# Optimization experiments

Measured on AMD Instinct MI355X. Metric: run time of the kernel, lower is better.

## Reference

```python
import jax, jax.numpy as jnp
import numpy as np

N = 50000
E = 800000
IN_C = 1024
HID = 64
HEADS = 4
OUT_C = 64
NEG_SLOPE = 0.2  # PyG GATConv default


def setup_inputs() -> dict:
    key = jax.random.key(0)
    ks = jax.random.split(key, 12)
    x = jax.random.normal(ks[0], (N, IN_C), dtype=jnp.float32)
    edge_index = jax.random.randint(ks[1], (2, E), 0, N, dtype=jnp.int64)
    s1 = 1.0 / np.sqrt(IN_C)
    s2 = 1.0 / np.sqrt(HEADS * HID)
    return {
        "x": x,
        "edge_index": edge_index,
        "W1": jax.random.normal(ks[2], (HEADS * HID, IN_C), dtype=jnp.float32) * s1,
        "a_src1": jax.random.normal(ks[3], (HEADS, HID), dtype=jnp.float32) * s2,
        "a_dst1": jax.random.normal(ks[4], (HEADS, HID), dtype=jnp.float32) * s2,
        "b1": jnp.zeros((HEADS * HID,), dtype=jnp.float32),
        "W2": jax.random.normal(ks[5], (OUT_C, HEADS * HID), dtype=jnp.float32) * s2,
        "a_src2": jax.random.normal(ks[6], (1, OUT_C), dtype=jnp.float32) * 0.1,
        "a_dst2": jax.random.normal(ks[7], (1, OUT_C), dtype=jnp.float32) * 0.1,
        "b2": jnp.zeros((OUT_C,), dtype=jnp.float32),
    }


def gat_conv(x, src, dst, W, a_src, a_dst, b, heads, concat):
    # x: [N, F_in]; src/dst: [E'] (self-loops already appended)
    n = x.shape[0]
    h = (x @ W.T).reshape(n, heads, -1)                 # [N, H, C]
    alpha_s = (h * a_src).sum(-1)                       # [N, H]
    alpha_d = (h * a_dst).sum(-1)                       # [N, H]
    e = jax.nn.leaky_relu(alpha_s[src] + alpha_d[dst], NEG_SLOPE)  # [E', H]
    # segment softmax over edges grouped by destination
    m = jax.ops.segment_max(e, dst, num_segments=n)     # [N, H]
    ex = jnp.exp(e - m[dst])
    denom = jax.ops.segment_sum(ex, dst, num_segments=n)
    alpha = ex / denom[dst]                             # [E', H]
    out = jax.ops.segment_sum(alpha[:, :, None] * h[src], dst, num_segments=n)  # [N, H, C]
    out = out.reshape(n, -1) if concat else out.mean(axis=1)
    return out + b


def reference(x, edge_index, W1, a_src1, a_dst1, b1, W2, a_src2, a_dst2, b2):
    n = x.shape[0]
    loop = jnp.arange(n, dtype=edge_index.dtype)
    src = jnp.concatenate([edge_index[0], loop])  # PyG add_self_loops=True
    dst = jnp.concatenate([edge_index[1], loop])
    # eval mode: dropout is identity
    h = gat_conv(x, src, dst, W1, a_src1, a_dst1, b1, HEADS, concat=True)
    h = jax.nn.elu(h)
    out = gat_conv(h, src, dst, W2, a_src2, a_dst2, b2, 1, concat=False)
    return out
```

## Files before the change

kernel.cpp:

```cpp
#include <hip/hip_runtime.h>
#include <hip/hip_bf16.h>
#include <math.h>

constexpr int IN_C = 1024;
constexpr int HEADS = 4;
constexpr int F1 = 256;
constexpr int OUT_C = 64;
constexpr float NEG = 0.2f;

using bf16x8 = __attribute__((ext_vector_type(8))) short;
using f32x4 = __attribute__((ext_vector_type(4))) float;

__device__ __forceinline__ float leaky(float x) { return x > 0.f ? x : NEG * x; }

__device__ __forceinline__ unsigned short bf16bits(float v) {
  __hip_bfloat16 b = __float2bfloat16(v);
  return *reinterpret_cast<unsigned short*>(&b);
}
__device__ __forceinline__ float bf2f(unsigned short u) {
  union { unsigned u; float f; } c; c.u = (unsigned)u << 16; return c.f;
}

#define GLD_LDS16(g, l)                                                        \
  __builtin_amdgcn_global_load_lds(                                            \
      (const __attribute__((address_space(1))) void*)(g),                      \
      (__attribute__((address_space(3))) void*)(l), 16, 0, 0)

__global__ void cvt_bf16_kernel(const float* __restrict__ in,
                                unsigned short* __restrict__ out, int n) {
  int i = blockIdx.x * blockDim.x + threadIdx.x;
  if (i < n) out[i] = bf16bits(in[i]);
}

constexpr int LDTA = 72;

__global__ __launch_bounds__(256, 2) void gemm1_mfma(const float* __restrict__ X,
                                                     const unsigned short* __restrict__ Wb,
                                                     unsigned short* __restrict__ Hb,
                                                     const float* __restrict__ a_src,
                                                     const float* __restrict__ a_dst,
                                                     float* __restrict__ as_out,
                                                     float* __restrict__ ad_out, int M) {
  __shared__ unsigned short As[64 * LDTA];
  __shared__ unsigned short Bs[256 * 64];
  const int tid = threadIdx.x;
  const int wave = tid >> 6;
  const int lane = tid & 63;
  const int m15 = lane & 15;
  const int q = lane >> 4;
  const int bm = blockIdx.x * 64;

  f32x4 acc[4][4];
#pragma unroll
  for (int i = 0; i < 4; ++i)
#pragma unroll
    for (int j = 0; j < 4; ++j) acc[i][j] = (f32x4){0.f, 0.f, 0.f, 0.f};

  const int ar = tid >> 2;
  const int acg = (tid & 3) * 16;
  const int agr = (bm + ar < M) ? (bm + ar) : (M - 1);
  const float* aptr = X + (size_t)agr * IN_C + acg;

  for (int kt = 0; kt < IN_C; kt += 64) {
    float4 a0 = *(const float4*)(aptr + kt + 0);
    float4 a1 = *(const float4*)(aptr + kt + 4);
    float4 a2 = *(const float4*)(aptr + kt + 8);
    float4 a3 = *(const float4*)(aptr + kt + 12);
#pragma unroll
    for (int p = 0; p < 8; ++p) {
      int s = p * 256 + tid;
      int r = s >> 3;
      int cb = s & 7;
      const unsigned short* g = Wb + (size_t)r * IN_C + kt + ((cb ^ (r & 7)) << 3);
      GLD_LDS16(g, &Bs[(p * 256 + wave * 64) * 8]);
    }
    union { uint4 u4[2]; __hip_bfloat162 h[8]; } pk;
    pk.h[0] = __float22bfloat162_rn(make_float2(a0.x, a0.y));
    pk.h[1] = __float22bfloat162_rn(make_float2(a0.z, a0.w));
    pk.h[2] = __float22bfloat162_rn(make_float2(a1.x, a1.y));
    pk.h[3] = __float22bfloat162_rn(make_float2(a1.z, a1.w));
    pk.h[4] = __float22bfloat162_rn(make_float2(a2.x, a2.y));
    pk.h[5] = __float22bfloat162_rn(make_float2(a2.z, a2.w));
    pk.h[6] = __float22bfloat162_rn(make_float2(a3.x, a3.y));
    pk.h[7] = __float22bfloat162_rn(make_float2(a3.z, a3.w));
    *(uint4*)&As[ar * LDTA + acg] = pk.u4[0];
    *(uint4*)&As[ar * LDTA + acg + 8] = pk.u4[1];
    __syncthreads();

#pragma unroll
    for (int k0 = 0; k0 < 64; k0 += 32) {
      bf16x8 af[4], bfr[4];
#pragma unroll
      for (int i = 0; i < 4; ++i)
        af[i] = *(const bf16x8*)&As[(i * 16 + m15) * LDTA + k0 + q * 8];
#pragma unroll
      for (int j = 0; j < 4; ++j) {
        int rb = wave * 64 + j * 16 + m15;
        int cbp = ((k0 >> 3) + q) ^ (rb & 7);
        bfr[j] = *(const bf16x8*)&Bs[rb * 64 + cbp * 8];
      }
#pragma unroll
      for (int i = 0; i < 4; ++i)
#pragma unroll
        for (int j = 0; j < 4; ++j)
          acc[i][j] = __builtin_amdgcn_mfma_f32_16x16x32_bf16(af[i], bfr[j], acc[i][j], 0, 0, 0);
    }
    __syncthreads();
  }
  float asf[4], adf[4];
#pragma unroll
  for (int j = 0; j < 4; ++j) {
    asf[j] = a_src[wave * 64 + j * 16 + m15];
    adf[j] = a_dst[wave * 64 + j * 16 + m15];
  }
#pragma unroll
  for (int i = 0; i < 4; ++i) {
#pragma unroll
    for (int r = 0; r < 4; ++r) {
      int row = bm + i * 16 + q * 4 + r;
      if (row < M) {
#pragma unroll
        for (int j = 0; j < 4; ++j)
          Hb[(size_t)row * F1 + wave * 64 + j * 16 + m15] = bf16bits(acc[i][j][r]);
      }
      float s = acc[i][0][r] * asf[0] + acc[i][1][r] * asf[1] +
                acc[i][2][r] * asf[2] + acc[i][3][r] * asf[3];
      float d = acc[i][0][r] * adf[0] + acc[i][1][r] * adf[1] +
                acc[i][2][r] * adf[2] + acc[i][3][r] * adf[3];
#pragma unroll
      for (int o = 1; o < 16; o <<= 1) {
        s += __shfl_xor(s, o, 64);
        d += __shfl_xor(d, o, 64);
      }
      if (m15 == 0 && row < M) {
        as_out[row * HEADS + wave] = s;
        ad_out[row * HEADS + wave] = d;
      }
    }
  }
}

__global__ __launch_bounds__(256, 4) void gemm2_mfma(const unsigned short* __restrict__ Y,
                                                     const unsigned short* __restrict__ W2b,
                                                     float* __restrict__ H2,
                                                     const float* __restrict__ a_src,
                                                     const float* __restrict__ a_dst,
                                                     float* __restrict__ as_out,
                                                     float* __restrict__ ad_out, int M) {
  __shared__ unsigned short As[64 * 64];
  __shared__ unsigned short Bs[64 * 64];
  const int tid = threadIdx.x;
  const int wave = tid >> 6;
  const int lane = tid & 63;
  const int m15 = lane & 15;
  const int q = lane >> 4;
  const int bm = blockIdx.x * 64;

  f32x4 acc[4];
#pragma unroll
  for (int j = 0; j < 4; ++j) acc[j] = (f32x4){0.f, 0.f, 0.f, 0.f};

  for (int kt = 0; kt < F1; kt += 64) {
#pragma unroll
    for (int p = 0; p < 2; ++p) {
      int s = p * 256 + tid;
      int r = s >> 3;
      int cb = s & 7;
      int colo = (cb ^ (r & 7)) << 3;
      int gr = (bm + r < M) ? (bm + r) : (M - 1);
      GLD_LDS16(Y + (size_t)gr * F1 + kt + colo, &As[(p * 256 + wave * 64) * 8]);
      GLD_LDS16(W2b + (size_t)r * F1 + kt + colo, &Bs[(p * 256 + wave * 64) * 8]);
    }
    __syncthreads();
#pragma unroll
    for (int k0 = 0; k0 < 64; k0 += 32) {
      int ra = wave * 16 + m15;
      bf16x8 af = *(const bf16x8*)&As[ra * 64 + ((((k0 >> 3) + q) ^ (ra & 7)) << 3)];
      bf16x8 bfr[4];
#pragma unroll
      for (int j = 0; j < 4; ++j) {
        int rb = j * 16 + m15;
        bfr[j] = *(const bf16x8*)&Bs[rb * 64 + ((((k0 >> 3) + q) ^ (rb & 7)) << 3)];
      }
#pragma unroll
      for (int j = 0; j < 4; ++j)
        acc[j] = __builtin_amdgcn_mfma_f32_16x16x32_bf16(af, bfr[j], acc[j], 0, 0, 0);
    }
    __syncthreads();
  }
  float asf[4], adf[4];
#pragma unroll
  for (int j = 0; j < 4; ++j) {
    asf[j] = a_src[j * 16 + m15];
    adf[j] = a_dst[j * 16 + m15];
  }
#pragma unroll
  for (int r = 0; r < 4; ++r) {
    int row = bm + wave * 16 + q * 4 + r;
    if (row < M) {
#pragma unroll
      for (int j = 0; j < 4; ++j) H2[(size_t)row * OUT_C + j * 16 + m15] = acc[j][r];
    }
    float s = acc[0][r] * asf[0] + acc[1][r] * asf[1] + acc[2][r] * asf[2] + acc[3][r] * asf[3];
    float d = acc[0][r] * adf[0] + acc[1][r] * adf[1] + acc[2][r] * adf[2] + acc[3][r] * adf[3];
#pragma unroll
    for (int o = 1; o < 16; o <<= 1) {
      s += __shfl_xor(s, o, 64);
      d += __shfl_xor(d, o, 64);
    }
    if (m15 == 0 && row < M) {
      as_out[row] = s;
      ad_out[row] = d;
    }
  }
}

__global__ void degree_kernel(const int* __restrict__ ei, int E, int N,
                              int* __restrict__ deg) {
  int e = blockIdx.x * blockDim.x + threadIdx.x;
  if (e >= E + N) return;
  int dst = (e < E) ? ei[E + e] : (e - E);
  atomicAdd(&deg[dst], 1);
}

__global__ __launch_bounds__(256) void scan_block_sums(const int* __restrict__ deg,
                                                       int* __restrict__ part, int n) {
  __shared__ int sm[256];
  int t = threadIdx.x;
  int i = blockIdx.x * 256 + t;
  sm[t] = (i < n) ? deg[i] : 0;
  __syncthreads();
  for (int off = 128; off > 0; off >>= 1) {
    if (t < off) sm[t] += sm[t + off];
    __syncthreads();
  }
  if (t == 0) part[blockIdx.x] = sm[0];
}

__global__ __launch_bounds__(256) void scan_partials(int* __restrict__ part, int P) {
  __shared__ int sm[256];
  int t = threadIdx.x;
  int v = (t < P) ? part[t] : 0;
  sm[t] = v;
  __syncthreads();
  for (int off = 1; off < 256; off <<= 1) {
    int u = (t >= off) ? sm[t - off] : 0;
    __syncthreads();
    sm[t] += u;
    __syncthreads();
  }
  if (t < P) part[t] = sm[t];
}

__global__ __launch_bounds__(256) void scan_final(const int* __restrict__ deg,
                                                  const int* __restrict__ part,
                                                  int* __restrict__ row_ptr, int n) {
  __shared__ int sm[256];
  int t = threadIdx.x;
  int i = blockIdx.x * 256 + t;
  sm[t] = (i < n) ? deg[i] : 0;
  __syncthreads();
  for (int off = 1; off < 256; off <<= 1) {
    int u = (t >= off) ? sm[t - off] : 0;
    __syncthreads();
    sm[t] += u;
    __syncthreads();
  }
  int base = blockIdx.x ? part[blockIdx.x - 1] : 0;
  if (i < n) row_ptr[i + 1] = base + sm[t];
  if (i == 0) row_ptr[0] = 0;
}

__global__ void scatter_kernel(const int* __restrict__ ei, int E, int N,
                               const int* __restrict__ row_ptr, int* __restrict__ fill,
                               int* __restrict__ col) {
  int e = blockIdx.x * blockDim.x + threadIdx.x;
  if (e >= E + N) return;
  int src, dst;
  if (e < E) { src = ei[e]; dst = ei[E + e]; }
  else       { src = e - E; dst = e - E; }
  int pos = row_ptr[dst] + atomicAdd(&fill[dst], 1);
  col[pos] = src;
}

__global__ __launch_bounds__(256) void agg1_kernel(const unsigned short* __restrict__ hb,
                                                   const float* __restrict__ as,
                                                   const float* __restrict__ ad,
                                                   const int* __restrict__ row_ptr,
                                                   const int* __restrict__ col,
                                                   const float* __restrict__ bias,
                                                   unsigned short* __restrict__ yb, int N) {
  int dst = (blockIdx.x * blockDim.x + threadIdx.x) >> 6;
  int lane = threadIdx.x & 63;
  if (dst >= N) return;
  const int s0 = row_ptr[dst], s1 = row_ptr[dst + 1];
  const int par = lane >> 5;
  const int cg = lane & 31;
  const int hh = cg >> 3;
  const float adl = ad[dst * 4 + hh];
  float acc[8];
#pragma unroll
  for (int k = 0; k < 8; ++k) acc[k] = 0.f;
  float den = 0.f;

  int i = s0 + par;
  for (; i + 2 < s1; i += 4) {
    int sA = col[i], sB = col[i + 2];
    float wA = __expf(leaky(as[sA * 4 + hh] + adl));
    float wB = __expf(leaky(as[sB * 4 + hh] + adl));
    uint4 hA = *(const uint4*)(hb + (size_t)sA * F1 + cg * 8);
    uint4 hB = *(const uint4*)(hb + (size_t)sB * F1 + cg * 8);
    den += wA + wB;
    const unsigned short* pa = (const unsigned short*)&hA;
    const unsigned short* pb = (const unsigned short*)&hB;
#pragma unroll
    for (int k = 0; k < 8; ++k) {
      acc[k] = fmaf(wA, bf2f(pa[k]), acc[k]);
      acc[k] = fmaf(wB, bf2f(pb[k]), acc[k]);
    }
  }
  for (; i < s1; i += 2) {
    int s = col[i];
    float w = __expf(leaky(as[s * 4 + hh] + adl));
    uint4 hv = *(const uint4*)(hb + (size_t)s * F1 + cg * 8);
    den += w;
    const unsigned short* p = (const unsigned short*)&hv;
#pragma unroll
    for (int k = 0; k < 8; ++k) acc[k] = fmaf(w, bf2f(p[k]), acc[k]);
  }
  den += __shfl_xor(den, 32, 64);
#pragma unroll
  for (int k = 0; k < 8; ++k) acc[k] += __shfl_xor(acc[k], 32, 64);

  if (par == 0) {
    const float iv = 1.f / den;
    float4 b0 = *(const float4*)(bias + cg * 8);
    float4 b1 = *(const float4*)(bias + cg * 8 + 4);
    float bv[8] = {b0.x, b0.y, b0.z, b0.w, b1.x, b1.y, b1.z, b1.w};
    ushort4 o[2];
    unsigned short* po = (unsigned short*)o;
#pragma unroll
    for (int k = 0; k < 8; ++k) {
      float v = acc[k] * iv + bv[k];
      v = v > 0.f ? v : (__expf(v) - 1.f);
      po[k] = bf16bits(v);
    }
    *(uint4*)(yb + (size_t)dst * F1 + cg * 8) = *(uint4*)o;
  }
}

__global__ __launch_bounds__(256) void agg2_kernel(const float* __restrict__ h,
                                                   const float* __restrict__ as,
                                                   const float* __restrict__ ad,
                                                   const int* __restrict__ row_ptr,
                                                   const int* __restrict__ col,
                                                   const float* __restrict__ bias,
                                                   float* __restrict__ out, int N) {
  int dst = (blockIdx.x * blockDim.x + threadIdx.x) >> 6;
  int lane = threadIdx.x & 63;
  if (dst >= N) return;
  const int s0 = row_ptr[dst], s1 = row_ptr[dst + 1];
  const int par = lane >> 5;
  const int cg = lane & 31;
  const float adl = ad[dst];
  float a0 = 0.f, a1 = 0.f, den = 0.f;

  int i = s0 + par;
  for (; i + 2 < s1; i += 4) {
    int sA = col[i], sB = col[i + 2];
    float wA = __expf(leaky(as[sA] + adl));
    float wB = __expf(leaky(as[sB] + adl));
    float2 hA = *(const float2*)(h + (size_t)sA * OUT_C + cg * 2);
    float2 hB = *(const float2*)(h + (size_t)sB * OUT_C + cg * 2);
    den += wA + wB;
    a0 = fmaf(wA, hA.x, a0); a1 = fmaf(wA, hA.y, a1);
    a0 = fmaf(wB, hB.x, a0); a1 = fmaf(wB, hB.y, a1);
  }
  for (; i < s1; i += 2) {
    int s = col[i];
    float w = __expf(leaky(as[s] + adl));
    float2 hv = *(const float2*)(h + (size_t)s * OUT_C + cg * 2);
    den += w;
    a0 = fmaf(w, hv.x, a0); a1 = fmaf(w, hv.y, a1);
  }
  den += __shfl_xor(den, 32, 64);
  a0 += __shfl_xor(a0, 32, 64);
  a1 += __shfl_xor(a1, 32, 64);
  if (par == 0) {
    const float iv = 1.f / den;
    float2 bv = *(const float2*)(bias + cg * 2);
    float2 o = make_float2(a0 * iv + bv.x, a1 * iv + bv.y);
    *(float2*)(out + (size_t)dst * OUT_C + cg * 2) = o;
  }
}

extern "C" void kernel_launch(void* const* d_in, const int* in_sizes, int n_in,
                              void* d_out, int out_size, void* d_ws, size_t ws_size,
                              hipStream_t stream) {
  const float* x      = (const float*)d_in[0];
  const int*   ei     = (const int*)d_in[1];
  const float* W1     = (const float*)d_in[2];
  const float* a_src1 = (const float*)d_in[3];
  const float* a_dst1 = (const float*)d_in[4];
  const float* b1     = (const float*)d_in[5];
  const float* W2     = (const float*)d_in[6];
  const float* a_src2 = (const float*)d_in[7];
  const float* a_dst2 = (const float*)d_in[8];
  const float* b2     = (const float*)d_in[9];
  float* out = (float*)d_out;

  const int N = in_sizes[0] / IN_C;
  const int E = in_sizes[1] / 2;
  const int ET = E + N;

  char* ws = (char*)d_ws;
  size_t off = 0;
  auto alloc = [&](size_t bytes) -> void* {
    void* p = ws + off;
    off = (off + bytes + 255) & ~(size_t)255;
    return p;
  };
  unsigned short* h1b = (unsigned short*)alloc((size_t)N * F1 * 2);
  unsigned short* y1b = (unsigned short*)alloc((size_t)N * F1 * 2);
  float* h2      = (float*)alloc((size_t)N * OUT_C * 4);
  float* as1     = (float*)alloc((size_t)N * HEADS * 4);
  float* ad1     = (float*)alloc((size_t)N * HEADS * 4);
  float* as2     = (float*)alloc((size_t)N * 4);
  float* ad2     = (float*)alloc((size_t)N * 4);
  int*   deg     = (int*)alloc((size_t)N * 4);
  int*   row_ptr = (int*)alloc((size_t)(N + 1) * 4);
  int*   fill    = (int*)alloc((size_t)N * 4);
  int*   col     = (int*)alloc((size_t)ET * 4);
  int*   part    = (int*)alloc(1024 * 4);
  unsigned short* W1b = (unsigned short*)alloc((size_t)F1 * IN_C * 2);
  unsigned short* W2b = (unsigned short*)alloc((size_t)OUT_C * F1 * 2);
  (void)off; (void)ws_size; (void)n_in; (void)out_size;

  hipMemsetAsync(deg, 0, (size_t)N * 4, stream);
  hipMemsetAsync(fill, 0, (size_t)N * 4, stream);

  cvt_bf16_kernel<<<(F1 * IN_C + 255) / 256, 256, 0, stream>>>(W1, W1b, F1 * IN_C);
  cvt_bf16_kernel<<<(OUT_C * F1 + 255) / 256, 256, 0, stream>>>(W2, W2b, OUT_C * F1);

  const int P = (N + 255) / 256;
  degree_kernel<<<(ET + 255) / 256, 256, 0, stream>>>(ei, E, N, deg);
  scan_block_sums<<<P, 256, 0, stream>>>(deg, part, N);
  scan_partials<<<1, 256, 0, stream>>>(part, P);
  scan_final<<<P, 256, 0, stream>>>(deg, part, row_ptr, N);
  scatter_kernel<<<(ET + 255) / 256, 256, 0, stream>>>(ei, E, N, row_ptr, fill, col);

  const int NB4 = (N + 3) / 4;

  gemm1_mfma<<<(N + 63) / 64, 256, 0, stream>>>(x, W1b, h1b, a_src1, a_dst1, as1, ad1, N);
  agg1_kernel<<<NB4, 256, 0, stream>>>(h1b, as1, ad1, row_ptr, col, b1, y1b, N);

  gemm2_mfma<<<(N + 63) / 64, 256, 0, stream>>>(y1b, W2b, h2, a_src2, a_dst2, as2, ad2, N);
  agg2_kernel<<<NB4, 256, 0, stream>>>(h2, as2, ad2, row_ptr, col, b2, out, N);
}
```

Before: 540.8 us.

## Fuse prep kernels, merge scan stages, unroll aggregation loops by four

Merges the two weight-to-bf16 conversions and the degree count into one prep kernel. Folds the partial-sum scan into the final scan, with each block summing its preceding partials by wave shuffles. Merges the two memsets into one by placing the fill counters next to the degree array. Adds a four-edge unrolled loop to both aggregation kernels so more gathers are in flight. This cuts launch count and per-launch overhead, in exchange for some redundant partial-sum work per block and higher register pressure in the aggregation kernels.

```diff
diff --git a/kernel.cpp b/kernel.cpp
--- a/kernel.cpp
+++ b/kernel.cpp
@@ -26,10 +26,29 @@
       (const __attribute__((address_space(1))) void*)(g),                      \
       (__attribute__((address_space(3))) void*)(l), 16, 0, 0)
 
-__global__ void cvt_bf16_kernel(const float* __restrict__ in,
-                                unsigned short* __restrict__ out, int n) {
-  int i = blockIdx.x * blockDim.x + threadIdx.x;
-  if (i < n) out[i] = bf16bits(in[i]);
+constexpr int NB_W1 = (F1 * IN_C) / 256;
+constexpr int NB_W2 = (OUT_C * F1) / 256;
+
+__global__ __launch_bounds__(256) void prep_kernel(const float* __restrict__ W1,
+                                                   unsigned short* __restrict__ W1b,
+                                                   const float* __restrict__ W2,
+                                                   unsigned short* __restrict__ W2b,
+                                                   const int* __restrict__ ei, int E, int N,
+                                                   int* __restrict__ deg) {
+  int b = blockIdx.x;
+  if (b < NB_W1) {
+    int i = b * 256 + threadIdx.x;
+    W1b[i] = bf16bits(W1[i]);
+  } else if (b < NB_W1 + NB_W2) {
+    int i = (b - NB_W1) * 256 + threadIdx.x;
+    W2b[i] = bf16bits(W2[i]);
+  } else {
+    int e = (b - NB_W1 - NB_W2) * 256 + threadIdx.x;
+    if (e < E + N) {
+      int dst = (e < E) ? ei[E + e] : (e - E);
+      atomicAdd(&deg[dst], 1);
+    }
+  }
 }
 
 constexpr int LDTA = 72;
@@ -215,14 +234,6 @@
   }
 }
 
-__global__ void degree_kernel(const int* __restrict__ ei, int E, int N,
-                              int* __restrict__ deg) {
-  int e = blockIdx.x * blockDim.x + threadIdx.x;
-  if (e >= E + N) return;
-  int dst = (e < E) ? ei[E + e] : (e - E);
-  atomicAdd(&deg[dst], 1);
-}
-
 __global__ __launch_bounds__(256) void scan_block_sums(const int* __restrict__ deg,
                                                        int* __restrict__ part, int n) {
   __shared__ int sm[256];
@@ -237,11 +248,18 @@
   if (t == 0) part[blockIdx.x] = sm[0];
 }
 
-__global__ __launch_bounds__(256) void scan_partials(int* __restrict__ part, int P) {
+__global__ __launch_bounds__(256) void scan_final2(const int* __restrict__ deg,
+                                                   const int* __restrict__ part,
+                                                   int* __restrict__ row_ptr, int n) {
   __shared__ int sm[256];
+  __shared__ int wsum[4];
   int t = threadIdx.x;
-  int v = (t < P) ? part[t] : 0;
-  sm[t] = v;
+  int i = blockIdx.x * 256 + t;
+  sm[t] = (i < n) ? deg[i] : 0;
+  int pv = (t < blockIdx.x) ? part[t] : 0;
+#pragma unroll
+  for (int o = 1; o < 64; o <<= 1) pv += __shfl_xor(pv, o, 64);
+  if ((t & 63) == 0) wsum[t >> 6] = pv;
   __syncthreads();
   for (int off = 1; off < 256; off <<= 1) {
     int u = (t >= off) ? sm[t - off] : 0;
@@ -249,24 +267,7 @@
     sm[t] += u;
     __syncthreads();
   }
-  if (t < P) part[t] = sm[t];
-}
-
-__global__ __launch_bounds__(256) void scan_final(const int* __restrict__ deg,
-                                                  const int* __restrict__ part,
-                                                  int* __restrict__ row_ptr, int n) {
-  __shared__ int sm[256];
-  int t = threadIdx.x;
-  int i = blockIdx.x * 256 + t;
-  sm[t] = (i < n) ? deg[i] : 0;
-  __syncthreads();
-  for (int off = 1; off < 256; off <<= 1) {
-    int u = (t >= off) ? sm[t - off] : 0;
-    __syncthreads();
-    sm[t] += u;
-    __syncthreads();
-  }
-  int base = blockIdx.x ? part[blockIdx.x - 1] : 0;
+  int base = wsum[0] + wsum[1] + wsum[2] + wsum[3];
   if (i < n) row_ptr[i + 1] = base + sm[t];
   if (i == 0) row_ptr[0] = 0;
 }
@@ -304,6 +305,29 @@
   float den = 0.f;
 
   int i = s0 + par;
+  for (; i + 6 < s1; i += 8) {
+    int sA = col[i], sB = col[i + 2], sC = col[i + 4], sD = col[i + 6];
+    float wA = __expf(leaky(as[sA * 4 + hh] + adl));
+    float wB = __expf(leaky(as[sB * 4 + hh] + adl));
+    float wC = __expf(leaky(as[sC * 4 + hh] + adl));
+    float wD = __expf(leaky(as[sD * 4 + hh] + adl));
+    uint4 hA = *(const uint4*)(hb + (size_t)sA * F1 + cg * 8);
+    uint4 hB = *(const uint4*)(hb + (size_t)sB * F1 + cg * 8);
+    uint4 hC = *(const uint4*)(hb + (size_t)sC * F1 + cg * 8);
+    uint4 hD = *(const uint4*)(hb + (size_t)sD * F1 + cg * 8);
+    den += (wA + wB) + (wC + wD);
+    const unsigned short* pa = (const unsigned short*)&hA;
+    const unsigned short* pb = (const unsigned short*)&hB;
+    const unsigned short* pc = (const unsigned short*)&hC;
+    const unsigned short* pd = (const unsigned short*)&hD;
+#pragma unroll
+    for (int k = 0; k < 8; ++k) {
+      acc[k] = fmaf(wA, bf2f(pa[k]), acc[k]);
+      acc[k] = fmaf(wB, bf2f(pb[k]), acc[k]);
+      acc[k] = fmaf(wC, bf2f(pc[k]), acc[k]);
+      acc[k] = fmaf(wD, bf2f(pd[k]), acc[k]);
+    }
+  }
   for (; i + 2 < s1; i += 4) {
     int sA = col[i], sB = col[i + 2];
     float wA = __expf(leaky(as[sA * 4 + hh] + adl));
@@ -366,6 +390,22 @@
   float a0 = 0.f, a1 = 0.f, den = 0.f;
 
   int i = s0 + par;
+  for (; i + 6 < s1; i += 8) {
+    int sA = col[i], sB = col[i + 2], sC = col[i + 4], sD = col[i + 6];
+    float wA = __expf(leaky(as[sA] + adl));
+    float wB = __expf(leaky(as[sB] + adl));
+    float wC = __expf(leaky(as[sC] + adl));
+    float wD = __expf(leaky(as[sD] + adl));
+    float2 hA = *(const float2*)(h + (size_t)sA * OUT_C + cg * 2);
+    float2 hB = *(const float2*)(h + (size_t)sB * OUT_C + cg * 2);
+    float2 hC = *(const float2*)(h + (size_t)sC * OUT_C + cg * 2);
+    float2 hD = *(const float2*)(h + (size_t)sD * OUT_C + cg * 2);
+    den += (wA + wB) + (wC + wD);
+    a0 = fmaf(wA, hA.x, a0); a1 = fmaf(wA, hA.y, a1);
+    a0 = fmaf(wB, hB.x, a0); a1 = fmaf(wB, hB.y, a1);
+    a0 = fmaf(wC, hC.x, a0); a1 = fmaf(wC, hC.y, a1);
+    a0 = fmaf(wD, hD.x, a0); a1 = fmaf(wD, hD.y, a1);
+  }
   for (; i + 2 < s1; i += 4) {
     int sA = col[i], sB = col[i + 2];
     float wA = __expf(leaky(as[sA] + adl));
@@ -427,27 +467,24 @@
   float* ad1     = (float*)alloc((size_t)N * HEADS * 4);
   float* as2     = (float*)alloc((size_t)N * 4);
   float* ad2     = (float*)alloc((size_t)N * 4);
-  int*   deg     = (int*)alloc((size_t)N * 4);
+  int*   deg     = (int*)alloc((size_t)N * 2 * 4);
+  int*   fill    = deg + N;
   int*   row_ptr = (int*)alloc((size_t)(N + 1) * 4);
-  int*   fill    = (int*)alloc((size_t)N * 4);
   int*   col     = (int*)alloc((size_t)ET * 4);
   int*   part    = (int*)alloc(1024 * 4);
   unsigned short* W1b = (unsigned short*)alloc((size_t)F1 * IN_C * 2);
   unsigned short* W2b = (unsigned short*)alloc((size_t)OUT_C * F1 * 2);
   (void)off; (void)ws_size; (void)n_in; (void)out_size;
 
-  hipMemsetAsync(deg, 0, (size_t)N * 4, stream);
-  hipMemsetAsync(fill, 0, (size_t)N * 4, stream);
-
-  cvt_bf16_kernel<<<(F1 * IN_C + 255) / 256, 256, 0, stream>>>(W1, W1b, F1 * IN_C);
-  cvt_bf16_kernel<<<(OUT_C * F1 + 255) / 256, 256, 0, stream>>>(W2, W2b, OUT_C * F1);
-
+  hipMemsetAsync(deg, 0, (size_t)N * 2 * 4, stream);
+
+  const int NBD = (ET + 255) / 256;
   const int P = (N + 255) / 256;
-  degree_kernel<<<(ET + 255) / 256, 256, 0, stream>>>(ei, E, N, deg);
+
+  prep_kernel<<<NB_W1 + NB_W2 + NBD, 256, 0, stream>>>(W1, W1b, W2, W2b, ei, E, N, deg);
   scan_block_sums<<<P, 256, 0, stream>>>(deg, part, N);
-  scan_partials<<<1, 256, 0, stream>>>(part, P);
-  scan_final<<<P, 256, 0, stream>>>(deg, part, row_ptr, N);
-  scatter_kernel<<<(ET + 255) / 256, 256, 0, stream>>>(ei, E, N, row_ptr, fill, col);
+  scan_final2<<<P, 256, 0, stream>>>(deg, part, row_ptr, N);
+  scatter_kernel<<<NBD, 256, 0, stream>>>(ei, E, N, row_ptr, fill, col);
 
   const int NB4 = (N + 3) / 4;
 
```

Result: faster. 522.9 us (-3.3%).
